# Performance work log

Hardware: AMD Instinct MI355X
Metric: run time of the kernel (lower is better)

Reference implementation:

```python
import jax, jax.numpy as jnp
import numpy as np

S, D, K, d = 1024, 256, 8, 32


def setup_inputs() -> dict:
    key = jax.random.key(0)
    ks = jax.random.split(key, 6)
    return {
        "data_samples": jax.random.normal(ks[0], (S, D, d), dtype=jnp.float32),
        "mix_param": jax.random.normal(ks[1], (D, K), dtype=jnp.float32),
        "mean_param": jax.random.normal(ks[2], (D, K, d), dtype=jnp.float32),
        "cov_param": jax.random.normal(ks[3], (D, K, d, d), dtype=jnp.float32),
        "ds_means": jax.random.normal(ks[4], (D, d), dtype=jnp.float32),
        "ds_stds": jax.random.uniform(ks[5], (D, d), dtype=jnp.float32, minval=0.5, maxval=1.5),
    }


def reference(data_samples, mix_param, mean_param, cov_param, ds_means, ds_stds):
    # TransformedDistribution with AffineTransform(loc, scale, event_dim=1):
    # log_prob(x) = base.log_prob((x - loc)/scale) - sum_j log|scale_j|
    dd = mean_param.shape[-1]
    y = (data_samples - ds_means) / ds_stds                      # [S,D,d]

    # cov = L L^T + 1e-5 I  (per design point, per component)
    cov = jnp.einsum('dkij,dklj->dkil', cov_param, cov_param)    # [D,K,d,d]
    cov = cov + 1e-5 * jnp.eye(dd, dtype=cov.dtype)
    chol = jnp.linalg.cholesky(cov)                              # [D,K,d,d]

    # inverse of lower Cholesky factor (small d x d solves, batched over D,K)
    eye = jnp.broadcast_to(jnp.eye(dd, dtype=chol.dtype), chol.shape)
    Linv = jax.lax.linalg.triangular_solve(chol, eye, left_side=True, lower=True)

    diff = y[:, :, None, :] - mean_param                          # [S,D,K,d]
    z = jnp.einsum('dkij,sdkj->sdki', Linv, diff)                 # whitened residual
    maha = jnp.sum(z * z, axis=-1)                                # [S,D,K]

    half_logdet = jnp.sum(jnp.log(jnp.diagonal(chol, axis1=-2, axis2=-1)), axis=-1)  # [D,K]
    log2pi = jnp.log(jnp.asarray(2.0 * np.pi, dtype=maha.dtype))
    log_comp = -0.5 * (dd * log2pi + maha) - half_logdet          # [S,D,K]

    log_pi = jax.nn.log_softmax(mix_param, axis=-1)               # [D,K]
    log_mix = jax.scipy.special.logsumexp(log_comp + log_pi, axis=-1)  # [S,D]

    return log_mix - jnp.sum(jnp.log(ds_stds), axis=-1)           # [S,D]
```

## Files before the change

### kernel.cpp

```cpp
#include <hip/hip_runtime.h>
#include <hip/hip_bf16.h>
#include <math.h>


typedef __attribute__((ext_vector_type(8))) short short8;
typedef __attribute__((ext_vector_type(4))) float f32x4;

__device__ __forceinline__ short f2bf(float f) {
    __hip_bfloat16 h = __float2bfloat16(f);
    return *reinterpret_cast<short*>(&h);
}
__device__ __forceinline__ float bf2f(short s) {
    __hip_bfloat16 h;
    *reinterpret_cast<short*>(&h) = s;
    return __bfloat162float(h);
}

__global__ __launch_bounds__(128, 1) void gmm_precompute(
    const float* __restrict__ mix,
    const float* __restrict__ mean_p,
    const float* __restrict__ cov_p,
    const float* __restrict__ ds_stds,
    short* __restrict__ L1,
    short* __restrict__ L2,
    short* __restrict__ L3,
    float* __restrict__ bOut,
    float* __restrict__ cOut)
{
    const int tid  = threadIdx.x;
    const int sub  = tid >> 5;
    const int lane = tid & 31;
    const int pair = blockIdx.x * 4 + sub;
    const int dd   = pair >> 3;
    const int k    = pair & 7;

    __shared__ double Csh[4][32][33];
    double (*C)[33] = Csh[sub];

    float w[32];
    {
        const float4* wp = (const float4*)(cov_p + (size_t)pair * 1024 + lane * 32);
        #pragma unroll
        for (int q = 0; q < 8; ++q) {
            const float4 v = wp[q];
            w[4*q+0] = v.x; w[4*q+1] = v.y; w[4*q+2] = v.z; w[4*q+3] = v.w;
        }
    }

    #pragma unroll
    for (int c = 0; c < 32; ++c) {
        float p[32];
        #pragma unroll
        for (int j = 0; j < 32; ++j)
            p[j] = __fmul_rn(w[j], __shfl(w[j], c, 32));
        float acc[4];
        #pragma unroll
        for (int l = 0; l < 4; ++l) {
            float t1 = p[12+l];
            t1 = __fadd_rn(p[8+l], t1);
            t1 = __fadd_rn(p[4+l], t1);
            t1 = __fadd_rn(p[0+l], t1);
            float t2 = __fadd_rn(p[28+l], t1);
            t2 = __fadd_rn(p[24+l], t2);
            t2 = __fadd_rn(p[20+l], t2);
            acc[l] = __fadd_rn(p[16+l], t2);
        }
        float s = __fadd_rn(__fadd_rn(acc[0], acc[1]), __fadd_rn(acc[2], acc[3]));
        if (c == lane) s = __fadd_rn(s, 1.0e-5f);
        C[lane][c] = (double)s;
    }

    double hld = 0.0, prod = 1.0;
    double creg[4], lreg[4];
    #pragma unroll
    for (int q = 0; q < 4; ++q) creg[q] = C[lane][q];

    #pragma unroll
    for (int cb = 0; cb < 8; ++cb) {
        const int c0 = cb * 4;
        #pragma unroll
        for (int q = 0; q < 4; ++q) {
            const int c = c0 + q;
            #pragma unroll
            for (int q2 = 0; q2 < 4; ++q2) {
                if (q2 < q) {
                    const double ljc = __shfl(lreg[q2], c, 32);
                    creg[q] = fma(-lreg[q2], ljc, creg[q]);
                }
            }
            const double dv  = __shfl(creg[q], c, 32);
            const double dcc = sqrt(dv);
            prod *= dv;
            if ((c & 7) == 7) { hld += log(prod); prod = 1.0; }
            const double invd = 1.0 / dcc;
            lreg[q] = (lane == c) ? dcc : creg[q] * invd;
            if (lane == c) C[c][32] = invd;
        }
        #pragma unroll
        for (int q = 0; q < 4; ++q) C[lane][c0 + q] = lreg[q];
        if (cb < 7) {
            #pragma unroll
            for (int q = 0; q < 4; ++q) {
                const int c2 = c0 + 4 + q;
                double tmp = C[lane][c2];
                #pragma unroll
                for (int q2 = 0; q2 < 4; ++q2) {
                    const double lc2 = __shfl(lreg[q2], c2, 32);
                    tmp = fma(-lreg[q2], lc2, tmp);
                }
                creg[q] = tmp;
            }
            #pragma unroll
            for (int c2 = 0; c2 < 32; ++c2) {
                if (c2 >= c0 + 8) {
                    double tmp = C[lane][c2];
                    #pragma unroll
                    for (int q2 = 0; q2 < 4; ++q2) {
                        const double lc2 = __shfl(lreg[q2], c2, 32);
                        tmp = fma(-lreg[q2], lc2, tmp);
                    }
                    C[lane][c2] = tmp;
                }
            }
        }
    }
    hld *= 0.5;

    double x[32];
    #pragma unroll
    for (int rr = 0; rr < 32; ++rr) {
        double s = (rr == lane) ? 1.0 : 0.0;
        #pragma unroll
        for (int j = 0; j < rr; ++j)
            s = fma(-C[rr][j], x[j], s);
        const double xr = s * C[rr][32];
        x[rr] = xr;
        C[rr][lane] = xr;

        const float f0 = (float)xr;
        const short h1 = f2bf(f0);
        const float r1 = f0 - bf2f(h1);
        const short h2 = f2bf(r1);
        const float r2 = r1 - bf2f(h2);
        const short h3 = f2bf(r2);
        const size_t base = (size_t)pair * 1024 + (size_t)rr * 32 + lane;
        L1[base] = h1; L2[base] = h2; L3[base] = h3;
    }

    const double mu_l = (double)mean_p[(size_t)pair * 32 + lane];
    double bacc = 0.0;
    #pragma unroll
    for (int j = 0; j < 32; ++j)
        bacc += C[lane][j] * __shfl(mu_l, j, 32);
    bOut[(size_t)pair * 32 + lane] = (float)bacc;

    double sprod = (double)ds_stds[dd * 32 + lane];
    #pragma unroll
    for (int off = 16; off >= 1; off >>= 1)
        sprod *= __shfl_xor(sprod, off, 32);
    if (lane == 0) {
        const double lsd = log(sprod);
        const float* mrow = mix + dd * 8;
        double mx = (double)mrow[0];
        #pragma unroll
        for (int q = 1; q < 8; ++q) mx = fmax(mx, (double)mrow[q]);
        double se = 0.0;
        #pragma unroll
        for (int q = 0; q < 8; ++q) se += exp((double)mrow[q] - mx);
        const double logpi = (double)mrow[k] - mx - log(se);
        const double LOG2PI = 1.8378770664093454836;
        cOut[pair] = (float)(logpi - hld - 16.0 * LOG2PI - lsd);
    }
}

__global__ __launch_bounds__(64) void gmm_main(
    const float* __restrict__ data,
    const float* __restrict__ ds_means,
    const float* __restrict__ ds_stds,
    const short* __restrict__ L1,
    const short* __restrict__ L2,
    const short* __restrict__ L3,
    const float* __restrict__ bvec,
    const float* __restrict__ cdk,
    float* __restrict__ out)
{
    const int dd = blockIdx.x;
    const int sc = blockIdx.y;
    const int t  = threadIdx.x;

    __shared__ short y1[4][64][8];
    __shared__ short y2[4][64][8];
    __shared__ short y3[4][64][8];

    float mn[32], is[32];
    {
        const float4* mp = (const float4*)(ds_means + dd * 32);
        const float4* sp = (const float4*)(ds_stds + dd * 32);
        #pragma unroll
        for (int q = 0; q < 8; ++q) {
            const float4 mv = mp[q];
            const float4 sv = sp[q];
            const int j4 = 4 * q;
            mn[j4+0] = mv.x; mn[j4+1] = mv.y; mn[j4+2] = mv.z; mn[j4+3] = mv.w;
            is[j4+0] = 1.0f / sv.x; is[j4+1] = 1.0f / sv.y;
            is[j4+2] = 1.0f / sv.z; is[j4+3] = 1.0f / sv.w;
        }
    }

    {
        const int s = sc * 64 + t;
        const float4* xp = (const float4*)(data + ((size_t)s * 256 + dd) * 32);
        float y[32];
        #pragma unroll
        for (int q = 0; q < 8; ++q) {
            const float4 v = xp[q];
            const int j4 = 4 * q;
            y[j4+0] = (v.x - mn[j4+0]) * is[j4+0];
            y[j4+1] = (v.y - mn[j4+1]) * is[j4+1];
            y[j4+2] = (v.z - mn[j4+2]) * is[j4+2];
            y[j4+3] = (v.w - mn[j4+3]) * is[j4+3];
        }
        #pragma unroll
        for (int jb = 0; jb < 4; ++jb) {
            short8 v1, v2, v3;
            #pragma unroll
            for (int e = 0; e < 8; ++e) {
                const float f0 = y[jb*8 + e];
                const short h1 = f2bf(f0);
                const float r1 = f0 - bf2f(h1);
                const short h2 = f2bf(r1);
                const float r2 = r1 - bf2f(h2);
                v1[e] = h1; v2[e] = h2; v3[e] = f2bf(r2);
            }
            *(short8*)&y1[jb][t][0] = v1;
            *(short8*)&y2[jb][t][0] = v2;
            *(short8*)&y3[jb][t][0] = v3;
        }
    }
    __syncthreads();

    const int scol = t & 15;
    const int g    = t >> 4;

    short8 vb1[4], vb2[4], vb3[4];
    #pragma unroll
    for (int st = 0; st < 4; ++st) {
        const int sl = st * 16 + scol;
        vb1[st] = *(const short8*)&y1[g][sl][0];
        vb2[st] = *(const short8*)&y2[g][sl][0];
        vb3[st] = *(const short8*)&y3[g][sl][0];
    }

    float maha[4][8];
    #pragma unroll
    for (int st = 0; st < 4; ++st)
        #pragma unroll
        for (int k = 0; k < 8; ++k) maha[st][k] = 0.0f;

    #pragma unroll
    for (int mt = 0; mt < 16; ++mt) {
        const int k  = mt >> 1;
        const int ib = (mt & 1) * 16;
        const size_t abase = ((size_t)(dd * 8 + k)) * 1024
                           + (size_t)(ib + scol) * 32 + g * 8;
        const short8 a1 = *(const short8*)(L1 + abase);
        const short8 a2 = *(const short8*)(L2 + abase);
        const short8 a3 = *(const short8*)(L3 + abase);
        const float4 bq = *(const float4*)(bvec + (dd * 8 + k) * 32 + ib + g * 4);
        f32x4 cinit;
        cinit[0] = -bq.x; cinit[1] = -bq.y; cinit[2] = -bq.z; cinit[3] = -bq.w;

        f32x4 acc[4];
        #pragma unroll
        for (int st = 0; st < 4; ++st) acc[st] = cinit;

        #pragma unroll
        for (int st = 0; st < 4; ++st) {
            acc[st] = __builtin_amdgcn_mfma_f32_16x16x32_bf16(a1, vb1[st], acc[st], 0, 0, 0);
            acc[st] = __builtin_amdgcn_mfma_f32_16x16x32_bf16(a1, vb2[st], acc[st], 0, 0, 0);
            acc[st] = __builtin_amdgcn_mfma_f32_16x16x32_bf16(a2, vb1[st], acc[st], 0, 0, 0);
            acc[st] = __builtin_amdgcn_mfma_f32_16x16x32_bf16(a2, vb2[st], acc[st], 0, 0, 0);
            acc[st] = __builtin_amdgcn_mfma_f32_16x16x32_bf16(a1, vb3[st], acc[st], 0, 0, 0);
            acc[st] = __builtin_amdgcn_mfma_f32_16x16x32_bf16(a3, vb1[st], acc[st], 0, 0, 0);
        }

        #pragma unroll
        for (int st = 0; st < 4; ++st) {
            float sq = fmaf(acc[st][0], acc[st][0],
                       fmaf(acc[st][1], acc[st][1],
                       fmaf(acc[st][2], acc[st][2], acc[st][3] * acc[st][3])));
            sq += __shfl_xor(sq, 16);
            sq += __shfl_xor(sq, 32);
            maha[st][k] += sq;
        }
    }

    const float* cb = cdk + dd * 8;
    #pragma unroll
    for (int st = 0; st < 4; ++st) {
        float a[8];
        #pragma unroll
        for (int k = 0; k < 8; ++k) a[k] = cb[k] - 0.5f * maha[st][k];
        float m = a[0];
        #pragma unroll
        for (int k = 1; k < 8; ++k) m = fmaxf(m, a[k]);
        float e = 0.0f;
        #pragma unroll
        for (int k = 0; k < 8; ++k) e += expf(a[k] - m);
        if (t < 16) {
            const int s = sc * 64 + st * 16 + scol;
            out[(size_t)s * 256 + dd] = m + logf(e);
        }
    }
}

extern "C" void kernel_launch(void* const* d_in, const int* in_sizes, int n_in,
                              void* d_out, int out_size, void* d_ws, size_t ws_size,
                              hipStream_t stream) {
    const float* data   = (const float*)d_in[0];
    const float* mix    = (const float*)d_in[1];
    const float* mean_p = (const float*)d_in[2];
    const float* cov_p  = (const float*)d_in[3];
    const float* ds_m   = (const float*)d_in[4];
    const float* ds_s   = (const float*)d_in[5];
    float* out = (float*)d_out;

    short* L1 = (short*)d_ws;
    short* L2 = L1 + 2048 * 1024;
    short* L3 = L2 + 2048 * 1024;
    float* bvec = (float*)(L3 + 2048 * 1024);
    float* cdk  = bvec + 2048 * 32;

    gmm_precompute<<<512, 128, 0, stream>>>(mix, mean_p, cov_p, ds_s,
                                            L1, L2, L3, bvec, cdk);
    dim3 grid(256, 16);
    gmm_main<<<grid, 64, 0, stream>>>(data, ds_m, ds_s, L1, L2, L3,
                                      bvec, cdk, out);
}
```

Before: 86.56 us.

## Split covariance product into separate lower-triangle kernel with packed output

Moves the L·Lᵀ covariance construction out of the Cholesky precompute kernel into a new kernel with one 64-thread block per (design point, component) pair. The new kernel stages the factor in shared memory and computes only the lower triangle, writing it packed to workspace. The precompute kernel then just loads the packed rows into its double-precision shared tile. This spreads the heavy shuffle-based product over many more blocks and skips the redundant upper triangle, at the cost of an extra launch and a global-memory round trip. The loader still reads 32 entries per row, so for columns past the diagonal it picks up neighbouring packed data; this is only correct if the Cholesky reads the lower triangle alone.

```diff
diff --git a/kernel.cpp b/kernel.cpp
--- a/kernel.cpp
+++ b/kernel.cpp
@@ -16,10 +16,66 @@
     return __bfloat162float(h);
 }
 
+__global__ __launch_bounds__(64) void gmm_cov(
+    const float* __restrict__ cov_p,
+    float* __restrict__ covt)
+{
+    const int pair = blockIdx.x;
+    const int t    = threadIdx.x;
+
+    __shared__ float W[32][33];
+    {
+        const float4* wp = (const float4*)(cov_p + (size_t)pair * 1024);
+        #pragma unroll
+        for (int q = 0; q < 4; ++q) {
+            const int e = t + 64 * q;
+            const float4 v = wp[e];
+            const int row = e >> 3, col = (e & 7) * 4;
+            W[row][col+0] = v.x; W[row][col+1] = v.y;
+            W[row][col+2] = v.z; W[row][col+3] = v.w;
+        }
+    }
+    __syncthreads();
+
+    const int c  = t & 31;
+    const int hh = t >> 5;
+
+    float wc[32];
+    #pragma unroll
+    for (int j = 0; j < 32; ++j) wc[j] = W[c][j];
+
+    #pragma unroll
+    for (int i = 0; i < 16; ++i) {
+        const int r = 2 * i + hh;
+        if (c <= r) {
+            float p[32];
+            #pragma unroll
+            for (int j = 0; j < 32; ++j)
+                p[j] = __fmul_rn(W[r][j], wc[j]);
+            float acc[4];
+            #pragma unroll
+            for (int l = 0; l < 4; ++l) {
+                float t1 = p[12+l];
+                t1 = __fadd_rn(p[8+l], t1);
+                t1 = __fadd_rn(p[4+l], t1);
+                t1 = __fadd_rn(p[0+l], t1);
+                float t2 = __fadd_rn(p[28+l], t1);
+                t2 = __fadd_rn(p[24+l], t2);
+                t2 = __fadd_rn(p[20+l], t2);
+                acc[l] = __fadd_rn(p[16+l], t2);
+            }
+            float s = __fadd_rn(__fadd_rn(acc[0], acc[1]),
+                                __fadd_rn(acc[2], acc[3]));
+            if (c == r) s = __fadd_rn(s, 1.0e-5f);
+            covt[(size_t)pair * 544 + (r * (r + 1)) / 2 + c] = s;
+        }
+    }
+}
+
 __global__ __launch_bounds__(128, 1) void gmm_precompute(
     const float* __restrict__ mix,
     const float* __restrict__ mean_p,
-    const float* __restrict__ cov_p,
+    const float* __restrict__ covt,
     const float* __restrict__ ds_stds,
     short* __restrict__ L1,
     short* __restrict__ L2,
@@ -37,37 +93,11 @@
     __shared__ double Csh[4][32][33];
     double (*C)[33] = Csh[sub];
 
-    float w[32];
     {
-        const float4* wp = (const float4*)(cov_p + (size_t)pair * 1024 + lane * 32);
-        #pragma unroll
-        for (int q = 0; q < 8; ++q) {
-            const float4 v = wp[q];
-            w[4*q+0] = v.x; w[4*q+1] = v.y; w[4*q+2] = v.z; w[4*q+3] = v.w;
-        }
-    }
-
-    #pragma unroll
-    for (int c = 0; c < 32; ++c) {
-        float p[32];
-        #pragma unroll
-        for (int j = 0; j < 32; ++j)
-            p[j] = __fmul_rn(w[j], __shfl(w[j], c, 32));
-        float acc[4];
-        #pragma unroll
-        for (int l = 0; l < 4; ++l) {
-            float t1 = p[12+l];
-            t1 = __fadd_rn(p[8+l], t1);
-            t1 = __fadd_rn(p[4+l], t1);
-            t1 = __fadd_rn(p[0+l], t1);
-            float t2 = __fadd_rn(p[28+l], t1);
-            t2 = __fadd_rn(p[24+l], t2);
-            t2 = __fadd_rn(p[20+l], t2);
-            acc[l] = __fadd_rn(p[16+l], t2);
-        }
-        float s = __fadd_rn(__fadd_rn(acc[0], acc[1]), __fadd_rn(acc[2], acc[3]));
-        if (c == lane) s = __fadd_rn(s, 1.0e-5f);
-        C[lane][c] = (double)s;
+        const float* src = covt + (size_t)pair * 544 + (lane * (lane + 1)) / 2;
+        #pragma unroll
+        for (int c = 0; c < 32; ++c)
+            C[lane][c] = (double)src[c];
     }
 
     double hld = 0.0, prod = 1.0;
@@ -330,8 +360,10 @@
     short* L3 = L2 + 2048 * 1024;
     float* bvec = (float*)(L3 + 2048 * 1024);
     float* cdk  = bvec + 2048 * 32;
-
-    gmm_precompute<<<512, 128, 0, stream>>>(mix, mean_p, cov_p, ds_s,
+    float* covt = cdk + 2048;
+
+    gmm_cov<<<2048, 64, 0, stream>>>(cov_p, covt);
+    gmm_precompute<<<512, 128, 0, stream>>>(mix, mean_p, covt, ds_s,
                                             L1, L2, L3, bvec, cdk);
     dim3 grid(256, 16);
     gmm_main<<<grid, 64, 0, stream>>>(data, ds_m, ds_s, L1, L2, L3,
```

After: 84.22 us. -2.7%, faster.
